# Kernel optimization log

Hardware: AMD Instinct MI355X
Metric: run time of the kernel (lower is better)

## Reference

```python
import jax, jax.numpy as jnp
import numpy as np

HIDDEN = 3584
NUM_HEADS = 28
NUM_KV_HEADS = 4
HEAD_DIM = 128
ROPE_THETA = 1000000.0


def setup_inputs() -> dict:
    key = jax.random.key(0)
    ks = jax.random.split(key, 12)
    B, S, C = 2, 1024, 3072
    inp = {
        "positions": jnp.arange(B * S, dtype=jnp.int32).reshape(B, S),
        "hidden_states": jax.random.normal(ks[0], (B, S, HIDDEN), dtype=jnp.float32),
        "k_cache": jax.random.normal(ks[1], (B, NUM_KV_HEADS, C, HEAD_DIM), dtype=jnp.float32),
        "v_cache": jax.random.normal(ks[2], (B, NUM_KV_HEADS, C, HEAD_DIM), dtype=jnp.float32),
        "cache_len": C,
        # torch Linear weights are [out_features, in_features]
        "q_w": jax.random.normal(ks[3], (NUM_HEADS * HEAD_DIM, HIDDEN), dtype=jnp.float32) * 0.02,
        "q_b": jax.random.normal(ks[4], (NUM_HEADS * HEAD_DIM,), dtype=jnp.float32) * 0.02,
        "k_w": jax.random.normal(ks[5], (NUM_KV_HEADS * HEAD_DIM, HIDDEN), dtype=jnp.float32) * 0.02,
        "k_b": jax.random.normal(ks[6], (NUM_KV_HEADS * HEAD_DIM,), dtype=jnp.float32) * 0.02,
        "v_w": jax.random.normal(ks[7], (NUM_KV_HEADS * HEAD_DIM, HIDDEN), dtype=jnp.float32) * 0.02,
        "v_b": jax.random.normal(ks[8], (NUM_KV_HEADS * HEAD_DIM,), dtype=jnp.float32) * 0.02,
        "o_w": jax.random.normal(ks[9], (HIDDEN, NUM_HEADS * HEAD_DIM), dtype=jnp.float32) * 0.02,
    }
    return inp


def _rope_cos_sin(positions, head_dim, base):
    # positions: [B,S] -> cos/sin [B,1,S,head_dim]
    inv_freq = 1.0 / (base ** (jnp.arange(0, head_dim, 2, dtype=jnp.float32) / head_dim))
    freqs = positions.astype(jnp.float32)[..., None] * inv_freq  # [B,S,D/2]
    emb = jnp.concatenate([freqs, freqs], axis=-1)               # [B,S,D]
    return jnp.cos(emb)[:, None], jnp.sin(emb)[:, None]


def _rotate_half(x):
    d = x.shape[-1] // 2
    return jnp.concatenate([-x[..., d:], x[..., :d]], axis=-1)


def reference(positions, hidden_states, k_cache, v_cache, cache_len,
              q_w, q_b, k_w, k_b, v_w, v_b, o_w):
    B, S, _ = hidden_states.shape
    scale = HEAD_DIM ** -0.5

    # QKV projections -> [B, H, S, D]
    q = (hidden_states @ q_w.T + q_b).reshape(B, S, NUM_HEADS, HEAD_DIM).transpose(0, 2, 1, 3)
    k = (hidden_states @ k_w.T + k_b).reshape(B, S, NUM_KV_HEADS, HEAD_DIM).transpose(0, 2, 1, 3)
    v = (hidden_states @ v_w.T + v_b).reshape(B, S, NUM_KV_HEADS, HEAD_DIM).transpose(0, 2, 1, 3)

    cos, sin = _rope_cos_sin(positions, HEAD_DIM, ROPE_THETA)
    q = q * cos + _rotate_half(q) * sin
    k = k * cos + _rotate_half(k) * sin

    # KV-cache concat (cache_len is static == full cache length here)
    k_full = jnp.concatenate([k_cache[:, :, :cache_len], k], axis=2)
    v_full = jnp.concatenate([v_cache[:, :, :cache_len], v], axis=2)
    new_k, new_v = k_full, v_full

    # GQA repeat: [B, Hkv, T, D] -> [B, H, T, D]
    groups = NUM_HEADS // NUM_KV_HEADS
    k_rep = jnp.repeat(k_full, groups, axis=1)
    v_rep = jnp.repeat(v_full, groups, axis=1)

    # Non-causal SDPA
    scores = jnp.einsum('bhqd,bhkd->bhqk', q, k_rep) * scale
    probs = jax.nn.softmax(scores, axis=-1)
    attn = jnp.einsum('bhqk,bhkd->bhqd', probs, v_rep)

    attn = attn.transpose(0, 2, 1, 3).reshape(B, S, NUM_HEADS * HEAD_DIM)
    out = attn @ o_w.T
    return out, new_k, new_v
```

## Files before the change

### kernel.cpp

```cpp
#include <hip/hip_runtime.h>
#include <hip/hip_bf16.h>
#include <math.h>

#define HIDDEN 3584
#define NHEADS 28
#define NKV 4
#define HDIM 128
#define BB 2
#define SS 1024
#define CC 3072
#define TT 4096
#define BS 2048
#define NQ 3584
#define GROUPS 7
#define SCALE 0.08838834764831845f
#define NT (HIDDEN / 32)
#define SM_OFF 16.0f

typedef unsigned short u16;
typedef __attribute__((ext_vector_type(4))) unsigned short u16x4;
typedef __attribute__((ext_vector_type(8))) unsigned short u16x8;
typedef __attribute__((ext_vector_type(8))) short s16x8;
typedef __attribute__((ext_vector_type(4))) float f32x4;

__device__ inline u16 f2bf(float x) {
  union { float f; unsigned int u; } v; v.f = x;
  unsigned int r = v.u + 0x7FFFu + ((v.u >> 16) & 1u);
  return (u16)(r >> 16);
}
__device__ inline unsigned int cvtpk(float lo, float hi) {
  unsigned int r;
  asm("v_cvt_pk_bf16_f32 %0, %1, %2" : "=v"(r) : "v"(lo), "v"(hi));
  return r;
}

__global__ __launch_bounds__(256) void copy_cache_kernel(
    const float4* __restrict__ kc, const float4* __restrict__ vc,
    float4* __restrict__ nk, float4* __restrict__ nv,
    u16* __restrict__ kbf, u16* __restrict__ vbft) {
  __shared__ u16 Tr[128][72];
  const int bh = blockIdx.y;
  const int t0 = blockIdx.x * 64;
  const int tid = threadIdx.x;
  #pragma unroll
  for (int i = 0; i < 8; ++i) {
    int idx = i * 256 + tid;
    int r = idx >> 5, c = idx & 31;
    size_t src = ((size_t)bh * CC + t0 + r) * 32 + c;
    size_t dst = ((size_t)bh * TT + t0 + r) * 32 + c;
    float4 k4 = kc[src], v4 = vc[src];
    nk[dst] = k4; nv[dst] = v4;
    u16x4 kb; kb[0] = f2bf(k4.x); kb[1] = f2bf(k4.y); kb[2] = f2bf(k4.z); kb[3] = f2bf(k4.w);
    *(u16x4*)(kbf + dst * 4) = kb;
    Tr[c * 4 + 0][r] = f2bf(v4.x);
    Tr[c * 4 + 1][r] = f2bf(v4.y);
    Tr[c * 4 + 2][r] = f2bf(v4.z);
    Tr[c * 4 + 3][r] = f2bf(v4.w);
  }
  __syncthreads();
  const int d = tid >> 1, half = tid & 1;
  const size_t obase = ((size_t)bh * 128 + d) * (size_t)TT + t0 + half * 32;
  #pragma unroll
  for (int i = 0; i < 4; ++i) {
    u16x8 v = *(const u16x8*)&Tr[d][half * 32 + i * 8];
    *(u16x8*)(vbft + obase + i * 8) = v;
  }
}

__global__ __launch_bounds__(256) void cvt_bf16_kernel(
    const float4* __restrict__ src, u16* __restrict__ dst, int n4) {
  int i = blockIdx.x * 256 + threadIdx.x;
  if (i < n4) {
    float4 v = src[i];
    u16x4 o; o[0] = f2bf(v.x); o[1] = f2bf(v.y); o[2] = f2bf(v.z); o[3] = f2bf(v.w);
    *(u16x4*)(dst + (size_t)i * 4) = o;
  }
}


__global__ __launch_bounds__(256) void gemm_qkv_bf_kernel(
    const u16* __restrict__ hbf, const u16* __restrict__ wbf,
    const float* __restrict__ qb, const float* __restrict__ kb,
    const float* __restrict__ vb, const int* __restrict__ pos,
    u16* __restrict__ qbf, float* __restrict__ nk, float* __restrict__ nv,
    u16* __restrict__ kbf, u16* __restrict__ vbft) {
  __shared__ u16 Ab[2][128 * 32];
  __shared__ u16 Bb[2][128 * 32];
  const int tid = threadIdx.x;
  const int w = tid >> 6, lane = tid & 63, lr = lane & 15, lg = lane >> 4;
  const int m0 = blockIdx.y * 128, n0 = blockIdx.x * 128;

  const bool isq = (n0 < NQ);
  const bool isk = (!isq) && (n0 < NQ + 512);
  const float* bias;
  if (isq)      bias = qb + n0;
  else if (isk) bias = kb + (n0 - NQ);
  else          bias = vb + (n0 - NQ - 512);

  f32x4 acc[2][8];
  #pragma unroll
  for (int f = 0; f < 2; ++f)
    #pragma unroll
    for (int n = 0; n < 8; ++n) acc[f][n] = (f32x4){0.f, 0.f, 0.f, 0.f};

  auto stageAB = [&](int buf, int k0) {
    #pragma unroll
    for (int i = 0; i < 2; ++i) {
      int ci = w * 128 + i * 64 + lane;
      int row = ci >> 2, c = ci & 3;
      __builtin_amdgcn_global_load_lds(
          (const __attribute__((address_space(1))) void*)(hbf + (size_t)(m0 + row) * HIDDEN + k0 + c * 8),
          (__attribute__((address_space(3))) void*)(&Ab[buf][(w * 128 + i * 64) * 8]),
          16, 0, 0);
      __builtin_amdgcn_global_load_lds(
          (const __attribute__((address_space(1))) void*)(wbf + (size_t)(n0 + row) * HIDDEN + k0 + c * 8),
          (__attribute__((address_space(3))) void*)(&Bb[buf][(w * 128 + i * 64) * 8]),
          16, 0, 0);
    }
  };

  stageAB(0, 0);
  __syncthreads();

  for (int kt = 0; kt < NT; ++kt) {
    const int cur = kt & 1;
    if (kt + 1 < NT) stageAB(cur ^ 1, (kt + 1) * 32);
    s16x8 af[2];
    af[0] = *(const s16x8*)&Ab[cur][(w * 32 + lr) * 32 + lg * 8];
    af[1] = *(const s16x8*)&Ab[cur][(w * 32 + 16 + lr) * 32 + lg * 8];
    #pragma unroll
    for (int n = 0; n < 8; ++n) {
      const s16x8 bf_ = *(const s16x8*)&Bb[cur][(n * 16 + lr) * 32 + lg * 8];
      acc[0][n] = __builtin_amdgcn_mfma_f32_16x16x32_bf16(af[0], bf_, acc[0][n], 0, 0, 0);
      acc[1][n] = __builtin_amdgcn_mfma_f32_16x16x32_bf16(af[1], bf_, acc[1][n], 0, 0, 0);
    }
    __syncthreads();
  }

  float bias_v[8];
  #pragma unroll
  for (int n = 0; n < 8; ++n) bias_v[n] = bias[n * 16 + lr];
  float invf[4];
  if (isq || isk) {
    #pragma unroll
    for (int n = 0; n < 4; ++n)
      invf[n] = __expf(-(float)(n * 16 + lr) * 0.21586735246819178f);
  }
  const int kvh = isq ? 0 : ((isk ? (n0 - NQ) : (n0 - NQ - 512)) >> 7);

  #pragma unroll
  for (int f = 0; f < 2; ++f)
    #pragma unroll
    for (int reg = 0; reg < 4; ++reg) {
      int m = m0 + w * 32 + f * 16 + lg * 4 + reg;
      float y[8];
      #pragma unroll
      for (int n = 0; n < 8; ++n) y[n] = acc[f][n][reg] + bias_v[n];
      if (isq || isk) {
        float p = (float)pos[m];
        #pragma unroll
        for (int n = 0; n < 4; ++n) {
          float sA, cA;
          __sincosf(p * invf[n], &sA, &cA);
          float lo = y[n], hi = y[n + 4];
          y[n]     = lo * cA - hi * sA;
          y[n + 4] = hi * cA + lo * sA;
        }
      }
      if (isq) {
        u16* dst = qbf + (size_t)m * NQ + n0;
        #pragma unroll
        for (int n = 0; n < 8; ++n) dst[n * 16 + lr] = f2bf(y[n] * SCALE);
      } else {
        int b_ = m >> 10, s_ = m & 1023;
        size_t rowoff = ((size_t)(b_ * NKV + kvh) * TT + CC + s_) * HDIM;
        if (isk) {
          #pragma unroll
          for (int n = 0; n < 8; ++n) {
            nk[rowoff + n * 16 + lr]  = y[n];
            kbf[rowoff + n * 16 + lr] = f2bf(y[n]);
          }
        } else {
          size_t vb0 = (size_t)(b_ * NKV + kvh) * 128;
          #pragma unroll
          for (int n = 0; n < 8; ++n) {
            nv[rowoff + n * 16 + lr] = y[n];
            vbft[(vb0 + n * 16 + lr) * (size_t)TT + CC + s_] = f2bf(y[n]);
          }
        }
      }
    }
}

__global__ __launch_bounds__(256) void gemm_out_bf_kernel(
    const u16* __restrict__ Abf, const u16* __restrict__ Wbf,
    float* __restrict__ Y) {
  __shared__ u16 Ab[2][128 * 32];
  __shared__ u16 Bb[2][128 * 32];
  const int tid = threadIdx.x;
  const int w = tid >> 6, lane = tid & 63, lr = lane & 15, lg = lane >> 4;
  const int m0 = blockIdx.y * 128, n0 = blockIdx.x * 128;

  f32x4 acc[2][8];
  #pragma unroll
  for (int f = 0; f < 2; ++f)
    #pragma unroll
    for (int n = 0; n < 8; ++n) acc[f][n] = (f32x4){0.f, 0.f, 0.f, 0.f};

  auto stageAB = [&](int buf, int k0) {
    #pragma unroll
    for (int i = 0; i < 2; ++i) {
      int ci = w * 128 + i * 64 + lane;
      int row = ci >> 2, c = ci & 3;
      __builtin_amdgcn_global_load_lds(
          (const __attribute__((address_space(1))) void*)(Abf + (size_t)(m0 + row) * HIDDEN + k0 + c * 8),
          (__attribute__((address_space(3))) void*)(&Ab[buf][(w * 128 + i * 64) * 8]),
          16, 0, 0);
      __builtin_amdgcn_global_load_lds(
          (const __attribute__((address_space(1))) void*)(Wbf + (size_t)(n0 + row) * HIDDEN + k0 + c * 8),
          (__attribute__((address_space(3))) void*)(&Bb[buf][(w * 128 + i * 64) * 8]),
          16, 0, 0);
    }
  };

  stageAB(0, 0);
  __syncthreads();

  for (int kt = 0; kt < NT; ++kt) {
    const int cur = kt & 1;
    if (kt + 1 < NT) stageAB(cur ^ 1, (kt + 1) * 32);
    s16x8 af[2];
    af[0] = *(const s16x8*)&Ab[cur][(w * 32 + lr) * 32 + lg * 8];
    af[1] = *(const s16x8*)&Ab[cur][(w * 32 + 16 + lr) * 32 + lg * 8];
    #pragma unroll
    for (int n = 0; n < 8; ++n) {
      const s16x8 bf_ = *(const s16x8*)&Bb[cur][(n * 16 + lr) * 32 + lg * 8];
      acc[0][n] = __builtin_amdgcn_mfma_f32_16x16x32_bf16(af[0], bf_, acc[0][n], 0, 0, 0);
      acc[1][n] = __builtin_amdgcn_mfma_f32_16x16x32_bf16(af[1], bf_, acc[1][n], 0, 0, 0);
    }
    __syncthreads();
  }

  #pragma unroll
  for (int f = 0; f < 2; ++f)
    #pragma unroll
    for (int reg = 0; reg < 4; ++reg) {
      int m = m0 + w * 32 + f * 16 + lg * 4 + reg;
      float* dst = Y + (size_t)m * NQ + n0;
      #pragma unroll
      for (int n = 0; n < 8; ++n) dst[n * 16 + lr] = acc[f][n][reg];
    }
}

__global__ __launch_bounds__(256) void gemm_qkv_kernel(
    const u16* __restrict__ hbf,
    const float* __restrict__ qw, const float* __restrict__ qb,
    const float* __restrict__ kw, const float* __restrict__ kb,
    const float* __restrict__ vw, const float* __restrict__ vb,
    const int* __restrict__ pos,
    u16* __restrict__ qbf, float* __restrict__ nk, float* __restrict__ nv,
    u16* __restrict__ kbf, u16* __restrict__ vbft) {
  __shared__ u16 Ab[2][128 * 32];
  __shared__ u16 Bb[2][128 * 32];
  const int tid = threadIdx.x;
  const int w = tid >> 6, lane = tid & 63, lr = lane & 15, lg = lane >> 4;
  const int m0 = blockIdx.y * 128, n0 = blockIdx.x * 128;

  const bool isq = (n0 < NQ);
  const bool isk = (!isq) && (n0 < NQ + 512);
  const float* Wb; const float* bias;
  if (isq)      { Wb = qw + (size_t)n0 * HIDDEN;          bias = qb + n0; }
  else if (isk) { Wb = kw + (size_t)(n0 - NQ) * HIDDEN;   bias = kb + (n0 - NQ); }
  else          { Wb = vw + (size_t)(n0 - NQ - 512) * HIDDEN; bias = vb + (n0 - NQ - 512); }

  f32x4 acc[2][8];
  #pragma unroll
  for (int f = 0; f < 2; ++f)
    #pragma unroll
    for (int n = 0; n < 8; ++n) acc[f][n] = (f32x4){0.f, 0.f, 0.f, 0.f};

  const int br = tid >> 1, bkh = (tid & 1) * 16;
  const float* Bsrc = Wb + (size_t)br * HIDDEN + bkh;

  auto stageA = [&](int buf, int k0) {
    #pragma unroll
    for (int i = 0; i < 2; ++i) {
      int ci = w * 128 + i * 64 + lane;
      int row = ci >> 2, c = ci & 3;
      __builtin_amdgcn_global_load_lds(
          (const __attribute__((address_space(1))) void*)(hbf + (size_t)(m0 + row) * HIDDEN + k0 + c * 8),
          (__attribute__((address_space(3))) void*)(&Ab[buf][(w * 128 + i * 64) * 8]),
          16, 0, 0);
    }
  };

  float4 fB[4];
  auto loadB = [&](int k0) {
    #pragma unroll
    for (int j = 0; j < 4; ++j) fB[j] = *(const float4*)(Bsrc + k0 + j * 4);
  };
  auto writeB = [&](int buf) {
    unsigned int pk[8];
    pk[0] = cvtpk(fB[0].x, fB[0].y); pk[1] = cvtpk(fB[0].z, fB[0].w);
    pk[2] = cvtpk(fB[1].x, fB[1].y); pk[3] = cvtpk(fB[1].z, fB[1].w);
    pk[4] = cvtpk(fB[2].x, fB[2].y); pk[5] = cvtpk(fB[2].z, fB[2].w);
    pk[6] = cvtpk(fB[3].x, fB[3].y); pk[7] = cvtpk(fB[3].z, fB[3].w);
    *(uint4*)&Bb[buf][br * 32 + bkh]     = make_uint4(pk[0], pk[1], pk[2], pk[3]);
    *(uint4*)&Bb[buf][br * 32 + bkh + 8] = make_uint4(pk[4], pk[5], pk[6], pk[7]);
  };

  stageA(0, 0); loadB(0); writeB(0);
  __syncthreads();

  for (int kt = 0; kt < NT; ++kt) {
    const int cur = kt & 1;
    if (kt + 1 < NT) { stageA(cur ^ 1, (kt + 1) * 32); loadB((kt + 1) * 32); }
    s16x8 af[2];
    af[0] = *(const s16x8*)&Ab[cur][(w * 32 + lr) * 32 + lg * 8];
    af[1] = *(const s16x8*)&Ab[cur][(w * 32 + 16 + lr) * 32 + lg * 8];
    #pragma unroll
    for (int n = 0; n < 8; ++n) {
      const s16x8 bf_ = *(const s16x8*)&Bb[cur][(n * 16 + lr) * 32 + lg * 8];
      acc[0][n] = __builtin_amdgcn_mfma_f32_16x16x32_bf16(af[0], bf_, acc[0][n], 0, 0, 0);
      acc[1][n] = __builtin_amdgcn_mfma_f32_16x16x32_bf16(af[1], bf_, acc[1][n], 0, 0, 0);
    }
    if (kt + 1 < NT) writeB(cur ^ 1);
    __syncthreads();
  }

  float bias_v[8];
  #pragma unroll
  for (int n = 0; n < 8; ++n) bias_v[n] = bias[n * 16 + lr];
  float invf[4];
  if (isq || isk) {
    #pragma unroll
    for (int n = 0; n < 4; ++n)
      invf[n] = __expf(-(float)(n * 16 + lr) * 0.21586735246819178f);
  }
  const int kvh = isq ? 0 : ((isk ? (n0 - NQ) : (n0 - NQ - 512)) >> 7);

  #pragma unroll
  for (int f = 0; f < 2; ++f)
    #pragma unroll
    for (int reg = 0; reg < 4; ++reg) {
      int m = m0 + w * 32 + f * 16 + lg * 4 + reg;
      float y[8];
      #pragma unroll
      for (int n = 0; n < 8; ++n) y[n] = acc[f][n][reg] + bias_v[n];
      if (isq || isk) {
        float p = (float)pos[m];
        #pragma unroll
        for (int n = 0; n < 4; ++n) {
          float sA, cA;
          __sincosf(p * invf[n], &sA, &cA);
          float lo = y[n], hi = y[n + 4];
          y[n]     = lo * cA - hi * sA;
          y[n + 4] = hi * cA + lo * sA;
        }
      }
      if (isq) {
        u16* dst = qbf + (size_t)m * NQ + n0;
        #pragma unroll
        for (int n = 0; n < 8; ++n) dst[n * 16 + lr] = f2bf(y[n] * SCALE);
      } else {
        int b_ = m >> 10, s_ = m & 1023;
        size_t rowoff = ((size_t)(b_ * NKV + kvh) * TT + CC + s_) * HDIM;
        if (isk) {
          #pragma unroll
          for (int n = 0; n < 8; ++n) {
            nk[rowoff + n * 16 + lr]  = y[n];
            kbf[rowoff + n * 16 + lr] = f2bf(y[n]);
          }
        } else {
          size_t vb0 = (size_t)(b_ * NKV + kvh) * 128;
          #pragma unroll
          for (int n = 0; n < 8; ++n) {
            nv[rowoff + n * 16 + lr] = y[n];
            vbft[(vb0 + n * 16 + lr) * (size_t)TT + CC + s_] = f2bf(y[n]);
          }
        }
      }
    }
}

__global__ __launch_bounds__(256) void gemm_out_kernel(
    const u16* __restrict__ Abf, const float* __restrict__ W,
    float* __restrict__ Y) {
  __shared__ u16 Ab[2][128 * 32];
  __shared__ u16 Bb[2][128 * 32];
  const int tid = threadIdx.x;
  const int w = tid >> 6, lane = tid & 63, lr = lane & 15, lg = lane >> 4;
  const int m0 = blockIdx.y * 128, n0 = blockIdx.x * 128;

  f32x4 acc[2][8];
  #pragma unroll
  for (int f = 0; f < 2; ++f)
    #pragma unroll
    for (int n = 0; n < 8; ++n) acc[f][n] = (f32x4){0.f, 0.f, 0.f, 0.f};

  const int br = tid >> 1, bkh = (tid & 1) * 16;
  const float* Bsrc = W + (size_t)(n0 + br) * HIDDEN + bkh;

  auto stageA = [&](int buf, int k0) {
    #pragma unroll
    for (int i = 0; i < 2; ++i) {
      int ci = w * 128 + i * 64 + lane;
      int row = ci >> 2, c = ci & 3;
      __builtin_amdgcn_global_load_lds(
          (const __attribute__((address_space(1))) void*)(Abf + (size_t)(m0 + row) * HIDDEN + k0 + c * 8),
          (__attribute__((address_space(3))) void*)(&Ab[buf][(w * 128 + i * 64) * 8]),
          16, 0, 0);
    }
  };

  float4 fB[4];
  auto loadB = [&](int k0) {
    #pragma unroll
    for (int j = 0; j < 4; ++j) fB[j] = *(const float4*)(Bsrc + k0 + j * 4);
  };
  auto writeB = [&](int buf) {
    unsigned int pk[8];
    pk[0] = cvtpk(fB[0].x, fB[0].y); pk[1] = cvtpk(fB[0].z, fB[0].w);
    pk[2] = cvtpk(fB[1].x, fB[1].y); pk[3] = cvtpk(fB[1].z, fB[1].w);
    pk[4] = cvtpk(fB[2].x, fB[2].y); pk[5] = cvtpk(fB[2].z, fB[2].w);
    pk[6] = cvtpk(fB[3].x, fB[3].y); pk[7] = cvtpk(fB[3].z, fB[3].w);
    *(uint4*)&Bb[buf][br * 32 + bkh]     = make_uint4(pk[0], pk[1], pk[2], pk[3]);
    *(uint4*)&Bb[buf][br * 32 + bkh + 8] = make_uint4(pk[4], pk[5], pk[6], pk[7]);
  };

  stageA(0, 0); loadB(0); writeB(0);
  __syncthreads();

  for (int kt = 0; kt < NT; ++kt) {
    const int cur = kt & 1;
    if (kt + 1 < NT) { stageA(cur ^ 1, (kt + 1) * 32); loadB((kt + 1) * 32); }
    s16x8 af[2];
    af[0] = *(const s16x8*)&Ab[cur][(w * 32 + lr) * 32 + lg * 8];
    af[1] = *(const s16x8*)&Ab[cur][(w * 32 + 16 + lr) * 32 + lg * 8];
    #pragma unroll
    for (int n = 0; n < 8; ++n) {
      const s16x8 bf_ = *(const s16x8*)&Bb[cur][(n * 16 + lr) * 32 + lg * 8];
      acc[0][n] = __builtin_amdgcn_mfma_f32_16x16x32_bf16(af[0], bf_, acc[0][n], 0, 0, 0);
      acc[1][n] = __builtin_amdgcn_mfma_f32_16x16x32_bf16(af[1], bf_, acc[1][n], 0, 0, 0);
    }
    if (kt + 1 < NT) writeB(cur ^ 1);
    __syncthreads();
  }

  #pragma unroll
  for (int f = 0; f < 2; ++f)
    #pragma unroll
    for (int reg = 0; reg < 4; ++reg) {
      int m = m0 + w * 32 + f * 16 + lg * 4 + reg;
      float* dst = Y + (size_t)m * NQ + n0;
      #pragma unroll
      for (int n = 0; n < 8; ++n) dst[n * 16 + lr] = acc[f][n][reg];
    }
}

__global__ __launch_bounds__(512, 2) void attn_kernel(
    const u16* __restrict__ qbf, const u16* __restrict__ kbf,
    const u16* __restrict__ vbft, u16* __restrict__ aout) {
  __shared__ __align__(16) u16 SMEM[53248];
  const int orig = blockIdx.x;
  const int swzb = (orig & 7) * 28 + (orig >> 3);
  const int g    = swzb / 28;
  const int ii   = swzb % 28;
  const int b    = g >> 2;
  const int hkv  = g & 3;
  const int h    = hkv * GROUPS + (ii >> 2);
  const int q0   = (ii & 3) * 256;

  const int tid  = threadIdx.x;
  const int w    = tid >> 6;
  const int quad = w >> 2;
  const int wq   = w & 3;
  const int lane = tid & 63;
  const int lr   = lane & 15;
  const int lg   = lane >> 4;
  const int qw0  = q0 + wq * 64;

  s16x8 qf[4][4];
  #pragma unroll
  for (int fq = 0; fq < 4; ++fq) {
    const u16* qp = qbf + (size_t)(b * SS + qw0 + fq * 16 + lr) * NQ + h * HDIM + lg * 8;
    #pragma unroll
    for (int kk = 0; kk < 4; ++kk) qf[fq][kk] = *(const s16x8*)(qp + kk * 32);
  }

  const size_t bh = (size_t)(b * NKV + hkv);
  const u16* kB = kbf  + bh * (size_t)TT * HDIM;
  const u16* vB = vbft + bh * (size_t)HDIM * TT;

  f32x4 oacc[4][8];
  #pragma unroll
  for (int fq = 0; fq < 4; ++fq)
    #pragma unroll
    for (int n = 0; n < 8; ++n) oacc[fq][n] = (f32x4){0.f, 0.f, 0.f, 0.f};
  float lsum[4] = {0.f, 0.f, 0.f, 0.f};

  u16* Ksq = SMEM + quad * 8192;
  u16* Vsq = SMEM + 16384 + quad * 8192;
  u16* Psw = SMEM + 32768 + w * 2560;

  auto stage = [&](int buf, int kt) {
    #pragma unroll
    for (int i = 0; i < 2; ++i) {
      int ci = (wq * 2 + i) * 64 + lane;
      int krow = ci >> 4, kc_ = ci & 15;
      const u16* ksrc = kB + (size_t)(kt * 32 + krow) * HDIM + ((kc_ ^ (krow & 7)) * 8);
      __builtin_amdgcn_global_load_lds(
          (const __attribute__((address_space(1))) void*)ksrc,
          (__attribute__((address_space(3))) void*)(Ksq + buf * 4096 + (wq * 2 + i) * 512),
          16, 0, 0);
      int vd = ci >> 2, vc_ = ci & 3;
      const u16* vsrc = vB + (size_t)vd * TT + kt * 32 + vc_ * 8;
      __builtin_amdgcn_global_load_lds(
          (const __attribute__((address_space(1))) void*)vsrc,
          (__attribute__((address_space(3))) void*)(Vsq + buf * 4096 + (wq * 2 + i) * 512),
          16, 0, 0);
    }
  };

  const int tbase = quad * 64;
  stage(0, tbase);
  __syncthreads();

  for (int it = 0; it < 64; ++it) {
    const int cur = it & 1;
    if (it + 1 < 64) stage(cur ^ 1, tbase + it + 1);

    f32x4 sacc[4][2];
    #pragma unroll
    for (int fq = 0; fq < 4; ++fq)
      #pragma unroll
      for (int n = 0; n < 2; ++n) sacc[fq][n] = (f32x4){0.f, 0.f, 0.f, 0.f};
    __builtin_amdgcn_s_setprio(1);
    #pragma unroll
    for (int kk = 0; kk < 4; ++kk) {
      #pragma unroll
      for (int n = 0; n < 2; ++n) {
        int row = n * 16 + lr;
        const s16x8 kf = *(const s16x8*)&Ksq[cur * 4096 + row * 128 + (((kk * 4 + lg) ^ (row & 7)) * 8)];
        #pragma unroll
        for (int fq = 0; fq < 4; ++fq)
          sacc[fq][n] = __builtin_amdgcn_mfma_f32_16x16x32_bf16(kf, qf[fq][kk], sacc[fq][n], 0, 0, 0);
      }
    }
    __builtin_amdgcn_s_setprio(0);

    #pragma unroll
    for (int fq = 0; fq < 4; ++fq) {
      #pragma unroll
      for (int n = 0; n < 2; ++n) {
        float p0 = __expf(sacc[fq][n][0] - SM_OFF);
        float p1 = __expf(sacc[fq][n][1] - SM_OFF);
        float p2 = __expf(sacc[fq][n][2] - SM_OFF);
        float p3 = __expf(sacc[fq][n][3] - SM_OFF);
        lsum[fq] += (p0 + p1) + (p2 + p3);
        uint2 pk = make_uint2(cvtpk(p0, p1), cvtpk(p2, p3));
        *(uint2*)&Psw[fq * 640 + lr * 40 + n * 16 + lg * 4] = pk;
      }
    }

    s16x8 pa[4];
    #pragma unroll
    for (int fq = 0; fq < 4; ++fq)
      pa[fq] = *(const s16x8*)&Psw[fq * 640 + lr * 40 + lg * 8];
    __builtin_amdgcn_s_setprio(1);
    #pragma unroll
    for (int n = 0; n < 8; ++n) {
      int row = n * 16 + lr;
      const s16x8 vf = *(const s16x8*)&Vsq[cur * 4096 + row * 32 + lg * 8];
      #pragma unroll
      for (int fq = 0; fq < 4; ++fq)
        oacc[fq][n] = __builtin_amdgcn_mfma_f32_16x16x32_bf16(pa[fq], vf, oacc[fq][n], 0, 0, 0);
    }
    __builtin_amdgcn_s_setprio(0);

    __syncthreads();
  }

  f32x4* OX = (f32x4*)SMEM;
  float* LX = (float*)(SMEM + 32768);
  #pragma unroll
  for (int half = 0; half < 2; ++half) {
    if (quad == 1) {
      #pragma unroll
      for (int fp = 0; fp < 2; ++fp) {
        int fq = half * 2 + fp;
        #pragma unroll
        for (int n = 0; n < 8; ++n)
          OX[(fp * 8 + n) * 256 + wq * 64 + lane] = oacc[fq][n];
      }
      if (half == 0) {
        #pragma unroll
        for (int fq = 0; fq < 4; ++fq) LX[fq * 256 + wq * 64 + lane] = lsum[fq];
      }
    }
    __syncthreads();
    if (quad == 0) {
      #pragma unroll
      for (int fp = 0; fp < 2; ++fp) {
        int fq = half * 2 + fp;
        #pragma unroll
        for (int n = 0; n < 8; ++n) {
          f32x4 v = OX[(fp * 8 + n) * 256 + wq * 64 + lane];
          oacc[fq][n] += v;
        }
      }
      if (half == 0) {
        #pragma unroll
        for (int fq = 0; fq < 4; ++fq) lsum[fq] += LX[fq * 256 + wq * 64 + lane];
      }
    }
    __syncthreads();
  }

  if (quad == 0) {
    #pragma unroll
    for (int fq = 0; fq < 4; ++fq) {
      float s = lsum[fq];
      s += __shfl_xor(s, 16);
      s += __shfl_xor(s, 32);
      #pragma unroll
      for (int reg = 0; reg < 4; ++reg) {
        int qrow = lg * 4 + reg;
        float invl = 1.f / __shfl(s, qrow);
        u16* orow = aout + (size_t)(b * SS + qw0 + fq * 16 + qrow) * NQ + h * HDIM;
        #pragma unroll
        for (int n = 0; n < 8; ++n)
          orow[n * 16 + lr] = f2bf(oacc[fq][n][reg] * invl);
      }
    }
  }
}

extern "C" void kernel_launch(void* const* d_in, const int* in_sizes, int n_in,
                              void* d_out, int out_size, void* d_ws, size_t ws_size,
                              hipStream_t stream) {
  const int*   positions = (const int*)d_in[0];
  const float* hidden    = (const float*)d_in[1];
  const float* kcache    = (const float*)d_in[2];
  const float* vcache    = (const float*)d_in[3];
  const float* qw = (const float*)d_in[5];
  const float* qb = (const float*)d_in[6];
  const float* kw = (const float*)d_in[7];
  const float* kb = (const float*)d_in[8];
  const float* vw = (const float*)d_in[9];
  const float* vb = (const float*)d_in[10];
  const float* ow = (const float*)d_in[11];

  float* out = (float*)d_out;
  float* nk  = out + (size_t)BS * NQ;
  float* nv  = nk + (size_t)BB * NKV * TT * HDIM;

  u16* qbf  = (u16*)d_ws;
  u16* kbf  = qbf + (size_t)BS * NQ;
  u16* vbft = kbf + (size_t)BB * NKV * TT * HDIM;
  u16* hbf  = vbft + (size_t)BB * NKV * HDIM * TT;
  u16* aws  = hbf;
  u16* wqkv = hbf + (size_t)BS * NQ;
  u16* owbf = wqkv;

  const size_t fast_need = ((size_t)BS * NQ * 2 + (size_t)BB * NKV * TT * HDIM * 2
                            + (size_t)(NQ + 1024) * HIDDEN) * sizeof(u16);
  const bool fast = ws_size >= fast_need;

  copy_cache_kernel<<<dim3(CC / 64, BB * NKV), 256, 0, stream>>>(
      (const float4*)kcache, (const float4*)vcache,
      (float4*)nk, (float4*)nv, kbf, vbft);
  cvt_bf16_kernel<<<(BS * HIDDEN / 4 + 255) / 256, 256, 0, stream>>>(
      (const float4*)hidden, hbf, BS * HIDDEN / 4);

  if (fast) {
    cvt_bf16_kernel<<<(NQ * HIDDEN / 4 + 255) / 256, 256, 0, stream>>>(
        (const float4*)qw, wqkv, NQ * HIDDEN / 4);
    cvt_bf16_kernel<<<(512 * HIDDEN / 4 + 255) / 256, 256, 0, stream>>>(
        (const float4*)kw, wqkv + (size_t)NQ * HIDDEN, 512 * HIDDEN / 4);
    cvt_bf16_kernel<<<(512 * HIDDEN / 4 + 255) / 256, 256, 0, stream>>>(
        (const float4*)vw, wqkv + (size_t)(NQ + 512) * HIDDEN, 512 * HIDDEN / 4);
    gemm_qkv_bf_kernel<<<dim3(36, 16), 256, 0, stream>>>(
        hbf, wqkv, qb, kb, vb, positions, qbf, nk, nv, kbf, vbft);
    cvt_bf16_kernel<<<(NQ * HIDDEN / 4 + 255) / 256, 256, 0, stream>>>(
        (const float4*)ow, owbf, NQ * HIDDEN / 4);
    attn_kernel<<<224, 512, 0, stream>>>(qbf, kbf, vbft, aws);
    gemm_out_bf_kernel<<<dim3(28, 16), 256, 0, stream>>>(aws, owbf, out);
  } else {
    gemm_qkv_kernel<<<dim3(36, 16), 256, 0, stream>>>(
        hbf, qw, qb, kw, kb, vw, vb, positions, qbf, nk, nv, kbf, vbft);
    attn_kernel<<<224, 512, 0, stream>>>(qbf, kbf, vbft, aws);
    gemm_out_kernel<<<dim3(28, 16), 256, 0, stream>>>(aws, ow, out);
  }
}
```

Measured before the change: 405.2 us.

## Permute K rows at staging so softmax probabilities stay in registers

K rows are loaded into shared memory in a permuted order, so the QK^T MFMA accumulator layout lines up directly with the A-operand layout needed by the PV MFMA. The probabilities are packed to bf16 in registers and fed straight into the PV MFMA, with no LDS write and read-back. This also shrinks the shared-memory allocation by dropping the per-wave P buffer. It depends on the permutation being exactly consistent with both MFMA layouts, which is easy to get wrong.

```diff
diff --git a/kernel.cpp b/kernel.cpp
--- a/kernel.cpp
+++ b/kernel.cpp
@@ -28,6 +28,10 @@
   unsigned int r = v.u + 0x7FFFu + ((v.u >> 16) & 1u);
   return (u16)(r >> 16);
 }
+__device__ inline float bf2f(u16 u) {
+  union { unsigned int i; float f; } v; v.i = ((unsigned int)u) << 16;
+  return v.f;
+}
 __device__ inline unsigned int cvtpk(float lo, float hi) {
   unsigned int r;
   asm("v_cvt_pk_bf16_f32 %0, %1, %2" : "=v"(r) : "v"(lo), "v"(hi));
@@ -76,7 +80,6 @@
     *(u16x4*)(dst + (size_t)i * 4) = o;
   }
 }
-
 
 __global__ __launch_bounds__(256) void gemm_qkv_bf_kernel(
     const u16* __restrict__ hbf, const u16* __restrict__ wbf,
@@ -461,7 +464,8 @@
 __global__ __launch_bounds__(512, 2) void attn_kernel(
     const u16* __restrict__ qbf, const u16* __restrict__ kbf,
     const u16* __restrict__ vbft, u16* __restrict__ aout) {
-  __shared__ __align__(16) u16 SMEM[53248];
+  __shared__ __align__(16) u16 SMEM[34816];
+
   const int orig = blockIdx.x;
   const int swzb = (orig & 7) * 28 + (orig >> 3);
   const int g    = swzb / 28;
@@ -501,14 +505,15 @@
 
   u16* Ksq = SMEM + quad * 8192;
   u16* Vsq = SMEM + 16384 + quad * 8192;
-  u16* Psw = SMEM + 32768 + w * 2560;
 
   auto stage = [&](int buf, int kt) {
     #pragma unroll
     for (int i = 0; i < 2; ++i) {
       int ci = (wq * 2 + i) * 64 + lane;
-      int krow = ci >> 4, kc_ = ci & 15;
-      const u16* ksrc = kB + (size_t)(kt * 32 + krow) * HDIM + ((kc_ ^ (krow & 7)) * 8);
+      int s = ci >> 4, kc_ = ci & 15;
+      int kv = (((s >> 3) & 1) << 4) | (((s >> 2) & 1) << 3)
+             | (((s >> 4) & 1) << 2) | (s & 3);
+      const u16* ksrc = kB + (size_t)(kt * 32 + kv) * HDIM + ((kc_ ^ (s & 7)) * 8);
       __builtin_amdgcn_global_load_lds(
           (const __attribute__((address_space(1))) void*)ksrc,
           (__attribute__((address_space(3))) void*)(Ksq + buf * 4096 + (wq * 2 + i) * 512),
@@ -549,24 +554,23 @@
     }
     __builtin_amdgcn_s_setprio(0);
 
+    s16x8 pa[4];
     #pragma unroll
     for (int fq = 0; fq < 4; ++fq) {
-      #pragma unroll
-      for (int n = 0; n < 2; ++n) {
-        float p0 = __expf(sacc[fq][n][0] - SM_OFF);
-        float p1 = __expf(sacc[fq][n][1] - SM_OFF);
-        float p2 = __expf(sacc[fq][n][2] - SM_OFF);
-        float p3 = __expf(sacc[fq][n][3] - SM_OFF);
-        lsum[fq] += (p0 + p1) + (p2 + p3);
-        uint2 pk = make_uint2(cvtpk(p0, p1), cvtpk(p2, p3));
-        *(uint2*)&Psw[fq * 640 + lr * 40 + n * 16 + lg * 4] = pk;
-      }
-    }
-
-    s16x8 pa[4];
-    #pragma unroll
-    for (int fq = 0; fq < 4; ++fq)
-      pa[fq] = *(const s16x8*)&Psw[fq * 640 + lr * 40 + lg * 8];
+      float p00 = __expf(sacc[fq][0][0] - SM_OFF);
+      float p01 = __expf(sacc[fq][0][1] - SM_OFF);
+      float p02 = __expf(sacc[fq][0][2] - SM_OFF);
+      float p03 = __expf(sacc[fq][0][3] - SM_OFF);
+      float p10 = __expf(sacc[fq][1][0] - SM_OFF);
+      float p11 = __expf(sacc[fq][1][1] - SM_OFF);
+      float p12 = __expf(sacc[fq][1][2] - SM_OFF);
+      float p13 = __expf(sacc[fq][1][3] - SM_OFF);
+      lsum[fq] += ((p00 + p01) + (p02 + p03)) + ((p10 + p11) + (p12 + p13));
+      uint4 pk4 = make_uint4(cvtpk(p00, p01), cvtpk(p02, p03),
+                             cvtpk(p10, p11), cvtpk(p12, p13));
+      pa[fq] = *(s16x8*)&pk4;
+    }
+
     __builtin_amdgcn_s_setprio(1);
     #pragma unroll
     for (int n = 0; n < 8; ++n) {
```

New measurement: 397.2 us. -2.0%, faster.
